# Kernel optimization log

Measured on AMD Instinct MI355X. Metric: run time of the kernel, lower is better.

The kernel has to match this reference:

```python
import jax, jax.numpy as jnp
import numpy as np

N_NODES = 50000
N_EDGES = 500000
IN_CH = 128
HID = 32
HEADS = 4
OUT_CH = 64
NEG_SLOPE = 0.2


def setup_inputs() -> dict:
    key = jax.random.key(0)
    ks = jax.random.split(key, 12)
    s = 0.1  # weight init scale
    x = jax.random.normal(ks[0], (N_NODES, IN_CH), jnp.float32)
    edge_index = jax.random.randint(ks[1], (2, N_EDGES), 0, N_NODES)
    # conv1: GATv2Conv(IN_CH, HID, heads=HEADS)
    W1l = jax.random.normal(ks[2], (IN_CH, HEADS * HID), jnp.float32) * s  # lin_l (source)
    W1r = jax.random.normal(ks[3], (IN_CH, HEADS * HID), jnp.float32) * s  # lin_r (target)
    att1 = jax.random.normal(ks[4], (HEADS, HID), jnp.float32) * s
    b1 = jnp.zeros((HEADS * HID,), jnp.float32)
    # conv2: GATv2Conv(HEADS*HID, OUT_CH, heads=1, concat=False)
    W2l = jax.random.normal(ks[5], (HEADS * HID, OUT_CH), jnp.float32) * s
    W2r = jax.random.normal(ks[6], (HEADS * HID, OUT_CH), jnp.float32) * s
    att2 = jax.random.normal(ks[7], (1, OUT_CH), jnp.float32) * s
    b2 = jnp.zeros((OUT_CH,), jnp.float32)
    return {"x": x, "edge_index": edge_index, "W1l": W1l, "W1r": W1r,
            "att1": att1, "b1": b1, "W2l": W2l, "W2r": W2r, "att2": att2, "b2": b2}


def gatv2_conv(x, src, dst, Wl, Wr, att, heads, ch, num_nodes):
    """GATv2Conv message passing. Returns [N, heads, ch] (pre-bias, pre-concat)."""
    xl = (x @ Wl).reshape(num_nodes, heads, ch)  # source transform
    xr = (x @ Wr).reshape(num_nodes, heads, ch)  # target transform
    xl_e = xl[src]                               # [E, H, C] gathered source feats
    m = jax.nn.leaky_relu(xl_e + xr[dst], NEG_SLOPE)
    score = jnp.einsum('ehc,hc->eh', m, att)     # [E, H]
    # segment softmax over incoming edges per destination node
    smax = jax.ops.segment_max(score, dst, num_segments=num_nodes)
    smax = jnp.where(jnp.isfinite(smax), smax, 0.0)
    p = jnp.exp(score - smax[dst])
    denom = jax.ops.segment_sum(p, dst, num_segments=num_nodes)
    alpha = p / (denom[dst] + 1e-16)
    out = jax.ops.segment_sum(alpha[:, :, None] * xl_e, dst, num_segments=num_nodes)
    return out


def reference(x, edge_index, W1l, W1r, att1, b1, W2l, W2r, att2, b2):
    n = x.shape[0]
    loop = jnp.arange(n, dtype=edge_index.dtype)
    src = jnp.concatenate([edge_index[0], loop])  # add self-loops (PyG default)
    dst = jnp.concatenate([edge_index[1], loop])
    # dropout(p=0.6) is identity in eval mode
    h = gatv2_conv(x, src, dst, W1l, W1r, att1, HEADS, HID, n)
    h = h.reshape(n, HEADS * HID) + b1            # concat=True
    h = jax.nn.elu(h)
    o = gatv2_conv(h, src, dst, W2l, W2r, att2, 1, OUT_CH, n)  # [N, 1, OUT]
    o = o + b2                                     # concat=False, heads=1 -> mean == identity
    return o[:, 0, :]
```

## Files before the change

kernel.cpp:

```cpp
#include <hip/hip_runtime.h>
#include <hip/hip_bf16.h>
#include <math.h>

#define N_NODESC 50000
#define N_EDGESC 500000
#define E_TOT    (N_EDGESC + N_NODESC)
#define IN_CH 128
#define HID 32
#define HEADS 4
#define HC (HEADS*HID)
#define OUT_CH 64
#define NEG_SLOPE 0.2f
#define NB_SCAN 196
#define N_STRIPS (N_NODESC/16)
#define NB_HIST 2149
#define NB_PREP 24
#define NB_SPLIT 6250

typedef unsigned short u16;
typedef __attribute__((ext_vector_type(8))) short short8;
typedef __attribute__((ext_vector_type(8))) unsigned short ushort8v;
typedef __attribute__((ext_vector_type(4))) float floatx4;

__device__ __forceinline__ u16 f2bf(float f){
  unsigned u = __float_as_uint(f);
  return (u16)((u + 0x7FFFu + ((u >> 16) & 1u)) >> 16);
}
__device__ __forceinline__ float bf2f(u16 b){ return __uint_as_float(((unsigned)b) << 16); }
__device__ __forceinline__ float lrelu(float v){ return fmaxf(v, NEG_SLOPE*v); }

__device__ __forceinline__ void edge_sd(const int* __restrict__ ei, int e, int& s, int& d){
  if (e < N_EDGESC){ s = ei[e]; d = ei[N_EDGESC + e]; }
  else { s = e - N_EDGESC; d = s; }
}

__global__ void k_misc(const int* __restrict__ ei, int* __restrict__ deg,
                       const float* __restrict__ X, u16* __restrict__ xhb,
                       const float* __restrict__ W1l, const float* __restrict__ W1r,
                       const float* __restrict__ W2l, const float* __restrict__ W2r,
                       u16* __restrict__ w1lh, u16* __restrict__ w1rh,
                       u16* __restrict__ w2lh, u16* __restrict__ w2rh){
  int b = blockIdx.x;
  if (b < NB_HIST){
    int e = b*256 + threadIdx.x;
    if (e < E_TOT){
      int s, d; edge_sd(ei, e, s, d);
      atomicAdd(&deg[d], 1);
    }
  } else if (b < NB_HIST + NB_PREP){
    int bb = b - NB_HIST;
    const float* W; u16 *Th; int N, base;
    if (bb < 8)      { W=W1l; Th=w1lh; N=HC;     base=bb;    }
    else if (bb < 16){ W=W1r; Th=w1rh; N=HC;     base=bb-8;  }
    else if (bb < 20){ W=W2l; Th=w2lh; N=OUT_CH; base=bb-16; }
    else             { W=W2r; Th=w2rh; N=OUT_CH; base=bb-20; }
    int tid = base*256 + threadIdx.x;
    int lane = tid & 63;
    int t = (tid >> 6) & 3;
    int c = tid >> 8;
    int k0 = t*32 + (lane>>4)*8;
    int n  = c*16 + (lane&15);
    #pragma unroll
    for (int j=0;j<8;j++){
      Th[(size_t)tid*8 + j] = f2bf(W[(size_t)(k0+j)*N + n]);
    }
  } else {
    int i = (b - NB_HIST - NB_PREP)*256 + threadIdx.x;
    if (i < N_NODESC*HC/4){
      float4 v = ((const float4*)X)[i];
      ushort4 h;
      h.x = f2bf(v.x); h.y = f2bf(v.y); h.z = f2bf(v.z); h.w = f2bf(v.w);
      ((ushort4*)xhb)[i] = h;
    }
  }
}

__global__ void k_scan_a(const int* __restrict__ deg, int* __restrict__ rs,
                         int* __restrict__ bsum){
  __shared__ int sh[256];
  int i = blockIdx.x*256 + threadIdx.x;
  int v = (i < N_NODESC) ? deg[i] : 0;
  sh[threadIdx.x] = v;
  __syncthreads();
  for (int off=1; off<256; off<<=1){
    int t = (threadIdx.x >= off) ? sh[threadIdx.x-off] : 0;
    __syncthreads();
    sh[threadIdx.x] += t;
    __syncthreads();
  }
  if (i < N_NODESC) rs[i] = sh[threadIdx.x] - v;
  if (threadIdx.x == 255) bsum[blockIdx.x] = sh[255];
}

__global__ void k_scan_bc(int* __restrict__ rs, const int* __restrict__ bsum,
                          int* __restrict__ cursor){
  __shared__ int sh[256];
  int v = (threadIdx.x < NB_SCAN) ? bsum[threadIdx.x] : 0;
  sh[threadIdx.x] = v;
  __syncthreads();
  for (int off=1; off<256; off<<=1){
    int t = (threadIdx.x >= off) ? sh[threadIdx.x-off] : 0;
    __syncthreads();
    sh[threadIdx.x] += t;
    __syncthreads();
  }
  int add = sh[blockIdx.x] - bsum[blockIdx.x];
  int i = blockIdx.x*256 + threadIdx.x;
  if (i < N_NODESC){
    int v2 = rs[i] + add;
    rs[i] = v2;
    cursor[i] = v2;
  }
}

__global__ void k_fill(const int* __restrict__ ei, int* __restrict__ cursor,
                       int* __restrict__ csrc){
  int e = blockIdx.x*blockDim.x + threadIdx.x;
  if (e >= E_TOT) return;
  int s, d; edge_sd(ei, e, s, d);
  int pos = atomicAdd(&cursor[d], 1);
  csrc[pos] = s;
}

template<int NCW, int SPB>
__launch_bounds__(256, 2)
__global__ void k_gemm_regB(const u16* __restrict__ Ab,
                            const u16* __restrict__ BlT, const u16* __restrict__ BrT,
                            u16* __restrict__ Olb, u16* __restrict__ Orb){
  constexpr int NLD = 2*NCW*16;
  int wave = threadIdx.x >> 6, lane = threadIdx.x & 63;
  int m = lane & 15, quad = lane >> 4;
  bool isl = (wave < 2);
  int ctbase = (isl ? wave : wave - 2) * NCW;
  const u16* __restrict__ BT = isl ? BlT : BrT;
  u16* __restrict__ Ob = isl ? Olb : Orb;

  short8 breg[NCW][4];
  #pragma unroll
  for (int c=0;c<NCW;c++)
    #pragma unroll
    for (int t=0;t<4;t++)
      breg[c][t] = *(const short8*)(BT + ((size_t)(((ctbase+c)*4 + t)*64) + lane)*8);

  int strip0 = blockIdx.x * SPB;
  short8 ah[2][4];

  {
    const u16* p1 = Ab + (size_t)(strip0*16 + m)*128 + quad*8;
    #pragma unroll
    for (int t=0;t<4;t++) ah[0][t] = *(const short8*)(p1 + t*32);
  }

  #pragma unroll
  for (int i=0;i<SPB;i++){
    int s = strip0 + i;
    if (s >= N_STRIPS) break;
    if (i+1 < SPB && s+1 < N_STRIPS){
      const u16* p1 = Ab + (size_t)((s+1)*16 + m)*128 + quad*8;
      #pragma unroll
      for (int t=0;t<4;t++) ah[(i+1)&1][t] = *(const short8*)(p1 + t*32);
    }
    const int b = i&1;
    floatx4 acc[NCW];
    #pragma unroll
    for (int c=0;c<NCW;c++) acc[c] = (floatx4){0.f,0.f,0.f,0.f};
    #pragma unroll
    for (int t=0;t<4;t++){
      #pragma unroll
      for (int c=0;c<NCW;c++)
        acc[c] = __builtin_amdgcn_mfma_f32_16x16x32_bf16(ah[b][t], breg[c][t], acc[c], 0,0,0);
    }
    int row0 = s*16;
    #pragma unroll
    for (int c=0;c<NCW;c++)
      #pragma unroll
      for (int r=0;r<4;r++)
        Ob[(size_t)(row0 + quad*4 + r)*NLD + (ctbase+c)*16 + m] = f2bf(acc[c][r]);
  }
}

__global__ void k_fused1(const int* __restrict__ rs, const int* __restrict__ deg,
                         const int* __restrict__ csrc, const u16* __restrict__ xlb,
                         const u16* __restrict__ xrb, const float* __restrict__ att,
                         const float* __restrict__ b1, u16* __restrict__ Hb){
  int wave = threadIdx.x >> 6;
  int lane = threadIdx.x & 63;
  int d = blockIdx.x*4 + wave;
  if (d >= N_NODESC) return;
  int g = lane >> 4;
  int l = lane & 15;

  float xrv[8], atv[8];
  {
    ushort8v xq = *(const ushort8v*)(xrb + (size_t)d*HC + 8*l);
    #pragma unroll
    for (int j=0;j<8;j++) xrv[j] = bf2f(xq[j]);
    float4 c = *(const float4*)(att + 8*l);
    float4 e = *(const float4*)(att + 8*l + 4);
    atv[0]=c.x; atv[1]=c.y; atv[2]=c.z; atv[3]=c.w;
    atv[4]=e.x; atv[5]=e.y; atv[6]=e.z; atv[7]=e.w;
  }

  int start = rs[d], degd = deg[d];

  float acc[8];
  #pragma unroll
  for (int j=0;j<8;j++) acc[j] = 0.f;
  float den = 0.f;

  for (int base = 0; base < degd; base += 64){
    int nb = degd - base; if (nb > 64) nb = 64;
    int idx = csrc[start + base + ((lane < nb) ? lane : 0)];
    for (int i = 0; i < nb; i += 4){
      bool valid = (i + g < nb);
      int s = __shfl(idx, i + g);
      ushort8v q = *(const ushort8v*)(xlb + (size_t)s*HC + 8*l);
      float xv[8];
      float sc = 0.f;
      #pragma unroll
      for (int j=0;j<8;j++){
        xv[j] = bf2f(q[j]);
        sc = fmaf(lrelu(xv[j] + xrv[j]), atv[j], sc);
      }
      sc += __shfl_xor(sc, 1);
      sc += __shfl_xor(sc, 2);
      float p = valid ? __expf(sc) : 0.f;
      den += p;
      #pragma unroll
      for (int j=0;j<8;j++) acc[j] = fmaf(p, xv[j], acc[j]);
    }
  }
  #pragma unroll
  for (int j=0;j<8;j++){
    acc[j] += __shfl_xor(acc[j], 16);
    acc[j] += __shfl_xor(acc[j], 32);
  }
  den += __shfl_xor(den, 16);
  den += __shfl_xor(den, 32);

  if (g == 0){
    float bv[8];
    float4 a = *(const float4*)(b1 + 8*l);
    float4 b = *(const float4*)(b1 + 8*l + 4);
    bv[0]=a.x; bv[1]=a.y; bv[2]=a.z; bv[3]=a.w;
    bv[4]=b.x; bv[5]=b.y; bv[6]=b.z; bv[7]=b.w;
    float inv = 1.f / (den + 1e-16f);
    u16 ohv[8];
    #pragma unroll
    for (int j=0;j<8;j++){
      float o = acc[j]*inv + bv[j];
      o = (o > 0.f) ? o : (__expf(o) - 1.f);
      ohv[j] = f2bf(o);
    }
    ushort4 h0 = {ohv[0],ohv[1],ohv[2],ohv[3]}, h1 = {ohv[4],ohv[5],ohv[6],ohv[7]};
    *(ushort4*)(Hb + (size_t)d*HC + 8*l)     = h0;
    *(ushort4*)(Hb + (size_t)d*HC + 8*l + 4) = h1;
  }
}

__global__ void k_fused2(const int* __restrict__ rs, const int* __restrict__ deg,
                         const int* __restrict__ csrc, const u16* __restrict__ xlb,
                         const u16* __restrict__ xrb, const float* __restrict__ att,
                         const float* __restrict__ b2, float* __restrict__ out){
  int wave = threadIdx.x >> 6;
  int lane = threadIdx.x & 63;
  int d = blockIdx.x*4 + wave;
  if (d >= N_NODESC) return;
  int g = lane >> 3;
  int l = lane & 7;

  float xrv[8], atv[8];
  {
    ushort8v xq = *(const ushort8v*)(xrb + (size_t)d*OUT_CH + 8*l);
    #pragma unroll
    for (int j=0;j<8;j++) xrv[j] = bf2f(xq[j]);
    float4 c = *(const float4*)(att + 8*l);
    float4 e = *(const float4*)(att + 8*l + 4);
    atv[0]=c.x; atv[1]=c.y; atv[2]=c.z; atv[3]=c.w;
    atv[4]=e.x; atv[5]=e.y; atv[6]=e.z; atv[7]=e.w;
  }

  int start = rs[d], degd = deg[d];

  float acc[8];
  #pragma unroll
  for (int j=0;j<8;j++) acc[j] = 0.f;
  float den = 0.f;

  for (int base = 0; base < degd; base += 64){
    int nb = degd - base; if (nb > 64) nb = 64;
    int idx = csrc[start + base + ((lane < nb) ? lane : 0)];
    for (int i = 0; i < nb; i += 8){
      bool valid = (i + g < nb);
      int s = __shfl(idx, i + g);
      ushort8v q = *(const ushort8v*)(xlb + (size_t)s*OUT_CH + 8*l);
      float xv[8];
      float sc = 0.f;
      #pragma unroll
      for (int j=0;j<8;j++){
        xv[j] = bf2f(q[j]);
        sc = fmaf(lrelu(xv[j] + xrv[j]), atv[j], sc);
      }
      sc += __shfl_xor(sc, 1);
      sc += __shfl_xor(sc, 2);
      sc += __shfl_xor(sc, 4);
      float p = valid ? __expf(sc) : 0.f;
      den += p;
      #pragma unroll
      for (int j=0;j<8;j++) acc[j] = fmaf(p, xv[j], acc[j]);
    }
  }
  #pragma unroll
  for (int j=0;j<8;j++){
    acc[j] += __shfl_xor(acc[j], 8);
    acc[j] += __shfl_xor(acc[j], 16);
    acc[j] += __shfl_xor(acc[j], 32);
  }
  den += __shfl_xor(den, 8);
  den += __shfl_xor(den, 16);
  den += __shfl_xor(den, 32);

  if (g == 0){
    float bv[8];
    float4 a = *(const float4*)(b2 + 8*l);
    float4 b = *(const float4*)(b2 + 8*l + 4);
    bv[0]=a.x; bv[1]=a.y; bv[2]=a.z; bv[3]=a.w;
    bv[4]=b.x; bv[5]=b.y; bv[6]=b.z; bv[7]=b.w;
    float inv = 1.f / (den + 1e-16f);
    float4 o0, o1;
    o0.x = acc[0]*inv + bv[0]; o0.y = acc[1]*inv + bv[1];
    o0.z = acc[2]*inv + bv[2]; o0.w = acc[3]*inv + bv[3];
    o1.x = acc[4]*inv + bv[4]; o1.y = acc[5]*inv + bv[5];
    o1.z = acc[6]*inv + bv[6]; o1.w = acc[7]*inv + bv[7];
    *(float4*)(out + (size_t)d*OUT_CH + 8*l)     = o0;
    *(float4*)(out + (size_t)d*OUT_CH + 8*l + 4) = o1;
  }
}

extern "C" void kernel_launch(void* const* d_in, const int* in_sizes, int n_in,
                              void* d_out, int out_size, void* d_ws, size_t ws_size,
                              hipStream_t stream) {
  const float* x    = (const float*)d_in[0];
  const int*   ei   = (const int*)d_in[1];
  const float* W1l  = (const float*)d_in[2];
  const float* W1r  = (const float*)d_in[3];
  const float* att1 = (const float*)d_in[4];
  const float* b1   = (const float*)d_in[5];
  const float* W2l  = (const float*)d_in[6];
  const float* W2r  = (const float*)d_in[7];
  const float* att2 = (const float*)d_in[8];
  const float* b2   = (const float*)d_in[9];
  float* out = (float*)d_out;

  float* ws = (float*)d_ws;
  size_t off = 0;
  u16* xl1b = (u16*)(ws + off); off += (size_t)N_NODESC*HC/2;
  u16* xr1b = (u16*)(ws + off); off += (size_t)N_NODESC*HC/2;
  u16* xl2b = (u16*)(ws + off); off += (size_t)N_NODESC*OUT_CH/2;
  u16* xr2b = (u16*)(ws + off); off += (size_t)N_NODESC*OUT_CH/2;
  u16* xhb  = (u16*)(ws + off); off += (size_t)N_NODESC*HC/2;
  u16* hb   = (u16*)(ws + off); off += (size_t)N_NODESC*HC/2;
  u16* w1lh = (u16*)(ws + off); off += IN_CH*HC/2;
  u16* w1rh = (u16*)(ws + off); off += IN_CH*HC/2;
  u16* w2lh = (u16*)(ws + off); off += HC*OUT_CH/2;
  u16* w2rh = (u16*)(ws + off); off += HC*OUT_CH/2;
  int* deg    = (int*)(ws + off); off += N_NODESC;
  int* rs     = (int*)(ws + off); off += N_NODESC;
  int* cursor = (int*)(ws + off); off += N_NODESC;
  int* bsum   = (int*)(ws + off); off += 256;
  int* csrc   = (int*)(ws + off); off += E_TOT;

  hipMemsetAsync(deg, 0, N_NODESC*sizeof(int), stream);
  k_misc<<<NB_HIST + NB_PREP + NB_SPLIT, 256, 0, stream>>>(
      ei, deg, x, xhb, W1l, W1r, W2l, W2r, w1lh, w1rh, w2lh, w2rh);
  k_scan_a<<<NB_SCAN, 256, 0, stream>>>(deg, rs, bsum);
  k_scan_bc<<<NB_SCAN, 256, 0, stream>>>(rs, bsum, cursor);
  k_fill<<<(E_TOT+255)/256, 256, 0, stream>>>(ei, cursor, csrc);

  const int NB_G = (N_STRIPS + 3)/4;
  k_gemm_regB<4,4><<<NB_G, 256, 0, stream>>>(xhb, w1lh, w1rh, xl1b, xr1b);
  k_fused1<<<(N_NODESC+3)/4, 256, 0, stream>>>(rs, deg, csrc, xl1b, xr1b, att1, b1, hb);

  k_gemm_regB<2,4><<<NB_G, 256, 0, stream>>>(hb, w2lh, w2rh, xl2b, xr2b);
  k_fused2<<<(N_NODESC+3)/4, 256, 0, stream>>>(rs, deg, csrc, xl2b, xr2b, att2, b2, out);
}
```

Baseline: 230.4 us.

## Fuse fp32-to-bf16 conversion into GEMM1 and merge with CSR fill; unroll gathers

Drops the separate pass that converts X to bf16 and instead converts fp32 rows on the fly inside the first-layer GEMM. That GEMM now shares one launch with the CSR fill kernel, with blocks split by index. This removes a full write and read of the bf16 copy of X plus one kernel launch. Both attention-aggregation kernels now process two edges per iteration, issuing two independent gathers to raise memory-level parallelism at the cost of more registers.

```diff
diff --git a/kernel.cpp b/kernel.cpp
--- a/kernel.cpp
+++ b/kernel.cpp
@@ -15,7 +15,7 @@
 #define N_STRIPS (N_NODESC/16)
 #define NB_HIST 2149
 #define NB_PREP 24
-#define NB_SPLIT 6250
+#define NB_GEMM1 782
 
 typedef unsigned short u16;
 typedef __attribute__((ext_vector_type(8))) short short8;
@@ -35,7 +35,6 @@
 }
 
 __global__ void k_misc(const int* __restrict__ ei, int* __restrict__ deg,
-                       const float* __restrict__ X, u16* __restrict__ xhb,
                        const float* __restrict__ W1l, const float* __restrict__ W1r,
                        const float* __restrict__ W2l, const float* __restrict__ W2r,
                        u16* __restrict__ w1lh, u16* __restrict__ w1rh,
@@ -47,7 +46,7 @@
       int s, d; edge_sd(ei, e, s, d);
       atomicAdd(&deg[d], 1);
     }
-  } else if (b < NB_HIST + NB_PREP){
+  } else {
     int bb = b - NB_HIST;
     const float* W; u16 *Th; int N, base;
     if (bb < 8)      { W=W1l; Th=w1lh; N=HC;     base=bb;    }
@@ -64,14 +63,6 @@
     for (int j=0;j<8;j++){
       Th[(size_t)tid*8 + j] = f2bf(W[(size_t)(k0+j)*N + n]);
     }
-  } else {
-    int i = (b - NB_HIST - NB_PREP)*256 + threadIdx.x;
-    if (i < N_NODESC*HC/4){
-      float4 v = ((const float4*)X)[i];
-      ushort4 h;
-      h.x = f2bf(v.x); h.y = f2bf(v.y); h.z = f2bf(v.z); h.w = f2bf(v.w);
-      ((ushort4*)xhb)[i] = h;
-    }
   }
 }
 
@@ -113,13 +104,76 @@
   }
 }
 
-__global__ void k_fill(const int* __restrict__ ei, int* __restrict__ cursor,
-                       int* __restrict__ csrc){
-  int e = blockIdx.x*blockDim.x + threadIdx.x;
-  if (e >= E_TOT) return;
-  int s, d; edge_sd(ei, e, s, d);
-  int pos = atomicAdd(&cursor[d], 1);
-  csrc[pos] = s;
+__launch_bounds__(256, 2)
+__global__ void k_fill_gemm1(const int* __restrict__ ei, int* __restrict__ cursor,
+                             int* __restrict__ csrc, const float* __restrict__ X,
+                             const u16* __restrict__ BlT, const u16* __restrict__ BrT,
+                             u16* __restrict__ Olb, u16* __restrict__ Orb){
+  int b = blockIdx.x;
+  if (b < NB_HIST){
+    int e = b*256 + threadIdx.x;
+    if (e < E_TOT){
+      int s, d; edge_sd(ei, e, s, d);
+      int pos = atomicAdd(&cursor[d], 1);
+      csrc[pos] = s;
+    }
+    return;
+  }
+  constexpr int NCW = 4, SPB = 4, NLD = 128;
+  int wave = threadIdx.x >> 6, lane = threadIdx.x & 63;
+  int m = lane & 15, quad = lane >> 4;
+  bool isl = (wave < 2);
+  int ctbase = (isl ? wave : wave - 2) * NCW;
+  const u16* __restrict__ BT = isl ? BlT : BrT;
+  u16* __restrict__ Ob = isl ? Olb : Orb;
+
+  short8 breg[NCW][4];
+  #pragma unroll
+  for (int c=0;c<NCW;c++)
+    #pragma unroll
+    for (int t=0;t<4;t++)
+      breg[c][t] = *(const short8*)(BT + ((size_t)(((ctbase+c)*4 + t)*64) + lane)*8);
+
+  int strip0 = (b - NB_HIST) * SPB;
+  short8 ah[2][4];
+
+  auto loadA = [&](int strip, int buf){
+    const float* p = X + (size_t)(strip*16 + m)*128 + quad*8;
+    #pragma unroll
+    for (int t=0;t<4;t++){
+      float4 f0 = *(const float4*)(p + t*32);
+      float4 f1 = *(const float4*)(p + t*32 + 4);
+      short8 a;
+      a[0]=f2bf(f0.x); a[1]=f2bf(f0.y); a[2]=f2bf(f0.z); a[3]=f2bf(f0.w);
+      a[4]=f2bf(f1.x); a[5]=f2bf(f1.y); a[6]=f2bf(f1.z); a[7]=f2bf(f1.w);
+      ah[buf][t] = a;
+    }
+  };
+
+  loadA(strip0, 0);
+
+  #pragma unroll
+  for (int i=0;i<SPB;i++){
+    int s = strip0 + i;
+    if (s >= N_STRIPS) break;
+    if (i+1 < SPB && s+1 < N_STRIPS) loadA(s+1, (i+1)&1);
+    const int bb = i&1;
+    floatx4 acc[NCW];
+    #pragma unroll
+    for (int c=0;c<NCW;c++) acc[c] = (floatx4){0.f,0.f,0.f,0.f};
+    #pragma unroll
+    for (int t=0;t<4;t++){
+      #pragma unroll
+      for (int c=0;c<NCW;c++)
+        acc[c] = __builtin_amdgcn_mfma_f32_16x16x32_bf16(ah[bb][t], breg[c][t], acc[c], 0,0,0);
+    }
+    int row0 = s*16;
+    #pragma unroll
+    for (int c=0;c<NCW;c++)
+      #pragma unroll
+      for (int r=0;r<4;r++)
+        Ob[(size_t)(row0 + quad*4 + r)*NLD + (ctbase+c)*16 + m] = f2bf(acc[c][r]);
+  }
 }
 
 template<int NCW, int SPB>
@@ -211,23 +265,35 @@
   for (int base = 0; base < degd; base += 64){
     int nb = degd - base; if (nb > 64) nb = 64;
     int idx = csrc[start + base + ((lane < nb) ? lane : 0)];
-    for (int i = 0; i < nb; i += 4){
-      bool valid = (i + g < nb);
-      int s = __shfl(idx, i + g);
-      ushort8v q = *(const ushort8v*)(xlb + (size_t)s*HC + 8*l);
-      float xv[8];
-      float sc = 0.f;
-      #pragma unroll
-      for (int j=0;j<8;j++){
-        xv[j] = bf2f(q[j]);
-        sc = fmaf(lrelu(xv[j] + xrv[j]), atv[j], sc);
+    for (int i = 0; i < nb; i += 8){
+      int e0 = i + g, e1 = i + 4 + g;
+      bool v0 = (e0 < nb), v1 = (e1 < nb);
+      int s0 = __shfl(idx, e0);
+      int s1 = __shfl(idx, e1);
+      ushort8v q0 = *(const ushort8v*)(xlb + (size_t)s0*HC + 8*l);
+      ushort8v q1 = *(const ushort8v*)(xlb + (size_t)s1*HC + 8*l);
+      {
+        float xv[8]; float sc = 0.f;
+        #pragma unroll
+        for (int j=0;j<8;j++){ xv[j] = bf2f(q0[j]); sc = fmaf(lrelu(xv[j]+xrv[j]), atv[j], sc); }
+        sc += __shfl_xor(sc, 1);
+        sc += __shfl_xor(sc, 2);
+        float p = v0 ? __expf(sc) : 0.f;
+        den += p;
+        #pragma unroll
+        for (int j=0;j<8;j++) acc[j] = fmaf(p, xv[j], acc[j]);
       }
-      sc += __shfl_xor(sc, 1);
-      sc += __shfl_xor(sc, 2);
-      float p = valid ? __expf(sc) : 0.f;
-      den += p;
-      #pragma unroll
-      for (int j=0;j<8;j++) acc[j] = fmaf(p, xv[j], acc[j]);
+      {
+        float xv[8]; float sc = 0.f;
+        #pragma unroll
+        for (int j=0;j<8;j++){ xv[j] = bf2f(q1[j]); sc = fmaf(lrelu(xv[j]+xrv[j]), atv[j], sc); }
+        sc += __shfl_xor(sc, 1);
+        sc += __shfl_xor(sc, 2);
+        float p = v1 ? __expf(sc) : 0.f;
+        den += p;
+        #pragma unroll
+        for (int j=0;j<8;j++) acc[j] = fmaf(p, xv[j], acc[j]);
+      }
     }
   }
   #pragma unroll
@@ -290,24 +356,37 @@
   for (int base = 0; base < degd; base += 64){
     int nb = degd - base; if (nb > 64) nb = 64;
     int idx = csrc[start + base + ((lane < nb) ? lane : 0)];
-    for (int i = 0; i < nb; i += 8){
-      bool valid = (i + g < nb);
-      int s = __shfl(idx, i + g);
-      ushort8v q = *(const ushort8v*)(xlb + (size_t)s*OUT_CH + 8*l);
-      float xv[8];
-      float sc = 0.f;
-      #pragma unroll
-      for (int j=0;j<8;j++){
-        xv[j] = bf2f(q[j]);
-        sc = fmaf(lrelu(xv[j] + xrv[j]), atv[j], sc);
+    for (int i = 0; i < nb; i += 16){
+      int e0 = i + g, e1 = i + 8 + g;
+      bool v0 = (e0 < nb), v1 = (e1 < nb);
+      int s0 = __shfl(idx, e0);
+      int s1 = __shfl(idx, e1);
+      ushort8v q0 = *(const ushort8v*)(xlb + (size_t)s0*OUT_CH + 8*l);
+      ushort8v q1 = *(const ushort8v*)(xlb + (size_t)s1*OUT_CH + 8*l);
+      {
+        float xv[8]; float sc = 0.f;
+        #pragma unroll
+        for (int j=0;j<8;j++){ xv[j] = bf2f(q0[j]); sc = fmaf(lrelu(xv[j]+xrv[j]), atv[j], sc); }
+        sc += __shfl_xor(sc, 1);
+        sc += __shfl_xor(sc, 2);
+        sc += __shfl_xor(sc, 4);
+        float p = v0 ? __expf(sc) : 0.f;
+        den += p;
+        #pragma unroll
+        for (int j=0;j<8;j++) acc[j] = fmaf(p, xv[j], acc[j]);
       }
-      sc += __shfl_xor(sc, 1);
-      sc += __shfl_xor(sc, 2);
-      sc += __shfl_xor(sc, 4);
-      float p = valid ? __expf(sc) : 0.f;
-      den += p;
-      #pragma unroll
-      for (int j=0;j<8;j++) acc[j] = fmaf(p, xv[j], acc[j]);
+      {
+        float xv[8]; float sc = 0.f;
+        #pragma unroll
+        for (int j=0;j<8;j++){ xv[j] = bf2f(q1[j]); sc = fmaf(lrelu(xv[j]+xrv[j]), atv[j], sc); }
+        sc += __shfl_xor(sc, 1);
+        sc += __shfl_xor(sc, 2);
+        sc += __shfl_xor(sc, 4);
+        float p = v1 ? __expf(sc) : 0.f;
+        den += p;
+        #pragma unroll
+        for (int j=0;j<8;j++) acc[j] = fmaf(p, xv[j], acc[j]);
+      }
     }
   }
   #pragma unroll
@@ -358,7 +437,6 @@
   u16* xr1b = (u16*)(ws + off); off += (size_t)N_NODESC*HC/2;
   u16* xl2b = (u16*)(ws + off); off += (size_t)N_NODESC*OUT_CH/2;
   u16* xr2b = (u16*)(ws + off); off += (size_t)N_NODESC*OUT_CH/2;
-  u16* xhb  = (u16*)(ws + off); off += (size_t)N_NODESC*HC/2;
   u16* hb   = (u16*)(ws + off); off += (size_t)N_NODESC*HC/2;
   u16* w1lh = (u16*)(ws + off); off += IN_CH*HC/2;
   u16* w1rh = (u16*)(ws + off); off += IN_CH*HC/2;
@@ -371,16 +449,16 @@
   int* csrc   = (int*)(ws + off); off += E_TOT;
 
   hipMemsetAsync(deg, 0, N_NODESC*sizeof(int), stream);
-  k_misc<<<NB_HIST + NB_PREP + NB_SPLIT, 256, 0, stream>>>(
-      ei, deg, x, xhb, W1l, W1r, W2l, W2r, w1lh, w1rh, w2lh, w2rh);
+  k_misc<<<NB_HIST + NB_PREP, 256, 0, stream>>>(
+      ei, deg, W1l, W1r, W2l, W2r, w1lh, w1rh, w2lh, w2rh);
   k_scan_a<<<NB_SCAN, 256, 0, stream>>>(deg, rs, bsum);
   k_scan_bc<<<NB_SCAN, 256, 0, stream>>>(rs, bsum, cursor);
-  k_fill<<<(E_TOT+255)/256, 256, 0, stream>>>(ei, cursor, csrc);
-
-  const int NB_G = (N_STRIPS + 3)/4;
-  k_gemm_regB<4,4><<<NB_G, 256, 0, stream>>>(xhb, w1lh, w1rh, xl1b, xr1b);
+
+  k_fill_gemm1<<<NB_HIST + NB_GEMM1, 256, 0, stream>>>(
+      ei, cursor, csrc, x, w1lh, w1rh, xl1b, xr1b);
+
   k_fused1<<<(N_NODESC+3)/4, 256, 0, stream>>>(rs, deg, csrc, xl1b, xr1b, att1, b1, hb);
 
-  k_gemm_regB<2,4><<<NB_G, 256, 0, stream>>>(hb, w2lh, w2rh, xl2b, xr2b);
+  k_gemm_regB<2,4><<<(N_STRIPS+3)/4, 256, 0, stream>>>(hb, w2lh, w2rh, xl2b, xr2b);
   k_fused2<<<(N_NODESC+3)/4, 256, 0, stream>>>(rs, deg, csrc, xl2b, xr2b, att2, b2, out);
 }
```

Measured after the change: 236.2 us. +2.5%, slower.
